# Performance work log

Hardware: AMD Instinct MI355X
Metric: run time of the kernel (lower is better)

Reference implementation:

```python
import jax, jax.numpy as jnp
import numpy as np

B = 4
G = 1024                      # GridSize
H = 1.0 / (G - 1)             # h = (right-left)/(GridSize-1), area=[[0,0],[1,1]]
GD = 0.0                      # boundary value for hard_encode padding


def _cross(a):
    # sum of 4-neighborhood: matches conv2d with kernel [[0,.5,0],[.5,0,.5],[0,.5,0]] / 0.5
    return a[..., :-2, 1:-1] + a[..., 2:, 1:-1] + a[..., 1:-1, :-2] + a[..., 1:-1, 2:]


def _inner(a):
    return a[..., 1:-1, 1:-1]


def kappa(x, mu):
    # assumed parameterization (kappa undefined in source): exp(mu * x)
    return jnp.exp(mu * x)


def setup_inputs() -> dict:
    key = jax.random.key(0)
    k1, k2, k3, k4 = jax.random.split(key, 4)
    pre = jax.random.normal(k1, (B, 1, G - 2, G - 2), jnp.float32)
    f = jax.random.normal(k2, (B, 1, G, G), jnp.float32)
    mu = jax.random.uniform(k3, (1,), jnp.float32)
    prev_pre = jax.random.normal(k4, (B, 1, G, G), jnp.float32) * 0.1
    return {"pre": pre, "f": f, "mu": mu, "prev_pre": prev_pre, "maxiter": 20}


def reference(pre, f, mu, prev_pre, maxiter):
    # w = kappa(prev_pre, mu) is iteration-invariant -> hoist out of the loop
    w = kappa(prev_pre, mu)            # [B,1,G,G]
    w_in = _inner(w)                   # [B,1,G-2,G-2]
    force = _inner(f) * (H * H)
    # k3 conv: 0.5*cross + 2*center
    y3 = 0.5 * _cross(w) + 2.0 * w_in

    def step(y, _):
        u = jnp.pad(y, ((0, 0), (0, 0), (1, 1), (1, 1)), constant_values=GD)
        y1 = 0.5 * _cross(u) * w_in    # conv(u, k1) * w_inner
        y2 = 0.5 * _cross(w * u)       # conv(w*u, k2)
        return (force + y1 + y2) / y3, None

    # original: one jac_step, then `maxiter` more -> maxiter+1 total
    y, _ = jax.lax.scan(step, pre, None, length=maxiter + 1)
    return y
```

## Files before the change

### kernel.cpp

```cpp
#include <hip/hip_runtime.h>

#define BB 4
#define GG 1024
#define NI 1022
#define SROW 1024
#define HH2 (2.0f / (1023.0f * 1023.0f))
#define OFFC 12
#define TOUTC 104
#define NTC 10

typedef float vf4 __attribute__((ext_vector_type(4)));
typedef float vf2 __attribute__((ext_vector_type(2)));

typedef __attribute__((address_space(3))) void lds_vt;
typedef const __attribute__((address_space(1))) void gm_vt;

__device__ __forceinline__ float dpp_left(float x) {
    int i = __builtin_bit_cast(int, x);
    i = __builtin_amdgcn_update_dpp(i, i, 0x138, 0xf, 0xf, false);
    return __builtin_bit_cast(float, i);
}
__device__ __forceinline__ float dpp_right(float x) {
    int i = __builtin_bit_cast(int, x);
    i = __builtin_amdgcn_update_dpp(i, i, 0x130, 0xf, 0xf, false);
    return __builtin_bit_cast(float, i);
}

#define WG_BAR() do { \
    asm volatile("s_waitcnt lgkmcnt(0)" ::: "memory"); \
    __builtin_amdgcn_s_barrier(); \
    asm volatile("" ::: "memory"); } while (0)

template<int TKP, int OFFR, int TOUTR, bool VIN4, bool VOUT4>
__global__ __launch_bounds__(512, 4)
void pinn_pipe(const float* __restrict__ ysrc,
               const float* __restrict__ fglob,
               const float* __restrict__ mu_p,
               const float* __restrict__ pp,
               float* __restrict__ yout)
{
    __shared__ __align__(16) float smem[20480];
    float* const wstg  = smem;
    float* const fstg  = smem + 8192;
    float* const ytopb = smem + 16384;
    float* const ybotb = smem + 18432;

    const int tid  = threadIdx.x;
    const int tx   = tid & 31, ty = tid >> 5;
    const int wvid = tid >> 6;
    const int ln   = tid & 63;
    const int b    = blockIdx.z;
    const int AR   = blockIdx.y * TOUTR - OFFR;
    const int R    = 4 * ty, c0 = 4 * tx;
    const float mu = mu_p[0];
    const size_t pb = (size_t)b * GG * GG;
    const int X    = AR + R;

    auto stage = [&](int A0) {
        const int scol = min(max(A0 + (ln & 31) * 4, 0), GG - 4);
        #pragma unroll
        for (int i = 0; i < 4; ++i) {
            const int j = (i * 8 + wvid) * 2 + (ln >> 5);
            const int g = min(max(AR + 1 + j, 0), GG - 1);
            const size_t go = pb + (size_t)g * GG + scol;
            __builtin_amdgcn_global_load_lds((gm_vt*)&pp[go],
                (lds_vt*)(wstg + (i * 8 + wvid) * 256), 16, 0, 0);
            __builtin_amdgcn_global_load_lds((gm_vt*)&fglob[go],
                (lds_vt*)(fstg + (i * 8 + wvid) * 256), 16, 0, 0);
        }
    };

    stage(2 * blockIdx.x * TOUTC - OFFC);

    const int tyo = ty * 128 + c0;
    const int upo = max(ty - 1, 0)  * 128 + c0;
    const int dno = min(ty + 1, 15) * 128 + c0;

    for (int tt = 0; tt < 2; ++tt) {
        const int A0 = (2 * blockIdx.x + tt) * TOUTC - OFFC;

        vf4 y0v, y1v, y2v, y3v;
        {
            const int i0 = min(max(X,     0), NI - 1);
            const int i1 = min(max(X + 1, 0), NI - 1);
            const int i2 = min(max(X + 2, 0), NI - 1);
            const int i3 = min(max(X + 3, 0), NI - 1);
            if (VIN4) {
                const int cy = min(max(A0 + c0, 0), SROW - 4);
                y0v = *(const vf4*)&ysrc[(size_t)(b * NI + i0) * SROW + cy];
                y1v = *(const vf4*)&ysrc[(size_t)(b * NI + i1) * SROW + cy];
                y2v = *(const vf4*)&ysrc[(size_t)(b * NI + i2) * SROW + cy];
                y3v = *(const vf4*)&ysrc[(size_t)(b * NI + i3) * SROW + cy];
            } else {
                const int cy  = min(max(A0 + c0, 0), NI - 2);
                const int cy2 = min(cy + 2, NI - 2);
                #define LDY(dst, ii) { \
                    const size_t base_ = (size_t)(b * NI + (ii)) * NI; \
                    const vf2 a_ = *(const vf2*)&ysrc[base_ + cy]; \
                    const vf2 b_ = *(const vf2*)&ysrc[base_ + cy2]; \
                    dst[0] = a_[0]; dst[1] = a_[1]; dst[2] = b_[0]; dst[3] = b_[1]; }
                LDY(y0v, i0) LDY(y1v, i1) LDY(y2v, i2) LDY(y3v, i3)
                #undef LDY
            }
        }

        __syncthreads();

        #pragma unroll
        for (int u = 0; u < 4; ++u) {
            vf4 w = *(const vf4*)&wstg[(R + u) * 128 + c0];
            #pragma unroll
            for (int m = 0; m < 4; ++m) w[m] = __expf(mu * w[m]);
            *(vf4*)&wstg[(R + u) * 128 + c0] = w;
        }
        __syncthreads();

        vf4 bN0,bS0,bW0,bE0,bf0, bN1,bS1,bW1,bE1,bf1,
            bN2,bS2,bW2,bE2,bf2, bN3,bS3,bW3,bE3,bf3;

        #define COEFF(kk, BN, BS, BW, BE, BF, YV) { \
            const int jN = max(R + (kk) - 1, 0); \
            const int jC = R + (kk); \
            const int jS = min(R + (kk) + 1, 63); \
            const int ce = min(c0 + 4, 124); \
            const vf4 n4 = *(const vf4*)&wstg[jN * 128 + c0]; \
            const vf2 n2 = *(const vf2*)&wstg[jN * 128 + ce]; \
            const vf4 c4 = *(const vf4*)&wstg[jC * 128 + c0]; \
            const vf2 c2 = *(const vf2*)&wstg[jC * 128 + ce]; \
            const vf4 s4 = *(const vf4*)&wstg[jS * 128 + c0]; \
            const vf2 s2 = *(const vf2*)&wstg[jS * 128 + ce]; \
            const vf4 wN = {n4[1], n4[2], n4[3], n2[0]}; \
            const vf4 wW = c4; \
            const vf4 wC = {c4[1], c4[2], c4[3], c2[0]}; \
            const vf4 wE = {c4[2], c4[3], c2[0], c2[1]}; \
            const vf4 wS = {s4[1], s4[2], s4[3], s2[0]}; \
            const vf4 aN = wC + wN, aS = wC + wS, aW = wC + wW, aE = wC + wE; \
            const vf4 den = (aN + aS) + (aW + aE); \
            const int gi = X + (kk); \
            vf4 rd; \
            _Pragma("unroll") \
            for (int m = 0; m < 4; ++m) { \
                float x = __builtin_amdgcn_rcpf(den[m]); \
                x = x * (2.0f - den[m] * x); \
                const int gj = A0 + c0 + m; \
                const bool in = (gi >= 0) && (gi < NI) && (gj >= 0) && (gj < NI); \
                rd[m] = in ? x : 0.0f; \
                YV[m] = in ? YV[m] : 0.0f; \
            } \
            BN = aN * rd; BS = aS * rd; BW = aW * rd; BE = aE * rd; \
            const vf4 f4 = *(const vf4*)&fstg[jC * 128 + c0]; \
            const float f1 = fstg[jC * 128 + min(c0 + 4, 127)]; \
            const vf4 fC = {f4[1], f4[2], f4[3], f1}; \
            BF = (fC * rd) * HH2; }

        COEFF(0, bN0,bS0,bW0,bE0,bf0, y0v)
        COEFF(1, bN1,bS1,bW1,bE1,bf1, y1v)
        COEFF(2, bN2,bS2,bW2,bE2,bf2, y2v)
        COEFF(3, bN3,bS3,bW3,bE3,bf3, y3v)
        #undef COEFF

        __syncthreads();

        if (tt == 0) stage((2 * blockIdx.x + 1) * TOUTC - OFFC);

        for (int t = 1; t <= TKP; ++t) {
            *(vf4*)&ytopb[tyo] = y0v;
            *(vf4*)&ybotb[tyo] = y3v;
            WG_BAR();
            const vf4 up = *(const vf4*)&ybotb[upo];
            const vf4 dn = *(const vf4*)&ytopb[dno];
            WG_BAR();
            const vf4 yW0 = {dpp_left(y0v[3]), y0v[0], y0v[1], y0v[2]};
            const vf4 yW1 = {dpp_left(y1v[3]), y1v[0], y1v[1], y1v[2]};
            const vf4 yW2 = {dpp_left(y2v[3]), y2v[0], y2v[1], y2v[2]};
            const vf4 yW3 = {dpp_left(y3v[3]), y3v[0], y3v[1], y3v[2]};
            const vf4 yE0 = {y0v[1], y0v[2], y0v[3], dpp_right(y0v[0])};
            const vf4 yE1 = {y1v[1], y1v[2], y1v[3], dpp_right(y1v[0])};
            const vf4 yE2 = {y2v[1], y2v[2], y2v[3], dpp_right(y2v[0])};
            const vf4 yE3 = {y3v[1], y3v[2], y3v[3], dpp_right(y3v[0])};
            vf4 n0 = bf0; n0 += bN0 * up;  n0 += bS0 * y1v; n0 += bW0 * yW0; n0 += bE0 * yE0;
            vf4 n1 = bf1; n1 += bN1 * y0v; n1 += bS1 * y2v; n1 += bW1 * yW1; n1 += bE1 * yE1;
            vf4 n2 = bf2; n2 += bN2 * y1v; n2 += bS2 * y3v; n2 += bW2 * yW2; n2 += bE2 * yE2;
            vf4 n3 = bf3; n3 += bN3 * y2v; n3 += bS3 * dn;  n3 += bW3 * yW3; n3 += bE3 * yE3;
            y0v = n0; y1v = n1; y2v = n2; y3v = n3;
        }

        if (c0 >= OFFC && c0 < OFFC + TOUTC) {
            const int gj0 = A0 + c0;
            if (VOUT4) {
                #define STORE4(kk, YV) { \
                    const int r = R + (kk); \
                    if (r >= OFFR && r < OFFR + TOUTR) { \
                        const int gi = AR + r; \
                        if (gi < NI && gj0 <= SROW - 4) \
                            *(vf4*)&yout[(size_t)(b * NI + gi) * SROW + gj0] = YV; } }
                STORE4(0, y0v) STORE4(1, y1v) STORE4(2, y2v) STORE4(3, y3v)
                #undef STORE4
            } else {
                #define STORE(kk, YV) { \
                    const int r = R + (kk); \
                    if (r >= OFFR && r < OFFR + TOUTR) { \
                        const int gi = AR + r; \
                        if (gi < NI) { \
                            const size_t rb = (size_t)(b * NI + gi) * NI; \
                            if (gj0 + 3 < NI) { \
                                vf2 pa, pv; pa[0]=YV[0]; pa[1]=YV[1]; pv[0]=YV[2]; pv[1]=YV[3]; \
                                *(vf2*)&yout[rb + gj0] = pa; *(vf2*)&yout[rb + gj0 + 2] = pv; \
                            } else { \
                                _Pragma("unroll") \
                                for (int m = 0; m < 4; ++m) \
                                    if (gj0 + m < NI) yout[rb + gj0 + m] = YV[m]; \
                            } \
                        } } }
                STORE(0, y0v) STORE(1, y1v) STORE(2, y2v) STORE(3, y3v)
                #undef STORE
            }
        }
    }
}

extern "C" void kernel_launch(void* const* d_in, const int* in_sizes, int n_in,
                              void* d_out, int out_size, void* d_ws, size_t ws_size,
                              hipStream_t stream) {
    const float* pre = (const float*)d_in[0];
    const float* f   = (const float*)d_in[1];
    const float* mu  = (const float*)d_in[2];
    const float* pp  = (const float*)d_in[3];

    float* yA = (float*)d_ws;

    const dim3 bs(512, 1, 1);
    pinn_pipe<11, 11, 42, false, true ><<<dim3(NTC/2, 25, BB), bs, 0, stream>>>(pre, f, mu, pp, yA);
    pinn_pipe<10, 10, 44, true,  false><<<dim3(NTC/2, 24, BB), bs, 0, stream>>>(yA,  f, mu, pp, (float*)d_out);
}
```

Before: 172.9 us.

## Compute exp coefficients in registers and recompute east coefficient per step

Removes the separate LDS pass that exponentiated the staged w tile and its extra barrier. Each thread now reads its own w rows, computes exp locally, and gets the neighbouring column through DPP lane shifts; the w staging is shifted by one row so the north row lines up. The east coefficient is no longer held in registers but rebuilt every iteration as mask minus the other three, which cuts four vf4 registers at the cost of extra ALU work in the hot loop. Exp is now computed redundantly for overlapping rows, and the iteration loop is reordered so fewer temporaries are live at once.

```diff
diff --git a/kernel.cpp b/kernel.cpp
--- a/kernel.cpp
+++ b/kernel.cpp
@@ -60,12 +60,14 @@
         const int scol = min(max(A0 + (ln & 31) * 4, 0), GG - 4);
         #pragma unroll
         for (int i = 0; i < 4; ++i) {
-            const int j = (i * 8 + wvid) * 2 + (ln >> 5);
-            const int g = min(max(AR + 1 + j, 0), GG - 1);
-            const size_t go = pb + (size_t)g * GG + scol;
-            __builtin_amdgcn_global_load_lds((gm_vt*)&pp[go],
+            const int j  = (i * 8 + wvid) * 2 + (ln >> 5);
+            const int gp = min(max(AR + j,     0), GG - 1);
+            const int gf = min(max(AR + 1 + j, 0), GG - 1);
+            __builtin_amdgcn_global_load_lds(
+                (gm_vt*)&pp[pb + (size_t)gp * GG + scol],
                 (lds_vt*)(wstg + (i * 8 + wvid) * 256), 16, 0, 0);
-            __builtin_amdgcn_global_load_lds((gm_vt*)&fglob[go],
+            __builtin_amdgcn_global_load_lds(
+                (gm_vt*)&fglob[pb + (size_t)gf * GG + scol],
                 (lds_vt*)(fstg + (i * 8 + wvid) * 256), 16, 0, 0);
         }
     };
@@ -76,8 +78,18 @@
     const int upo = max(ty - 1, 0)  * 128 + c0;
     const int dno = min(ty + 1, 15) * 128 + c0;
 
+    vf4 rmv;
+    #pragma unroll
+    for (int k = 0; k < 4; ++k)
+        rmv[k] = ((unsigned)(X + k) < (unsigned)NI) ? 1.0f : 0.0f;
+
     for (int tt = 0; tt < 2; ++tt) {
         const int A0 = (2 * blockIdx.x + tt) * TOUTC - OFFC;
+
+        vf4 colm;
+        #pragma unroll
+        for (int m = 0; m < 4; ++m)
+            colm[m] = ((unsigned)(A0 + c0 + m) < (unsigned)NI) ? 1.0f : 0.0f;
 
         vf4 y0v, y1v, y2v, y3v;
         {
@@ -106,57 +118,52 @@
 
         __syncthreads();
 
-        #pragma unroll
-        for (int u = 0; u < 4; ++u) {
-            vf4 w = *(const vf4*)&wstg[(R + u) * 128 + c0];
-            #pragma unroll
-            for (int m = 0; m < 4; ++m) w[m] = __expf(mu * w[m]);
-            *(vf4*)&wstg[(R + u) * 128 + c0] = w;
-        }
-        __syncthreads();
-
-        vf4 bN0,bS0,bW0,bE0,bf0, bN1,bS1,bW1,bE1,bf1,
-            bN2,bS2,bW2,bE2,bf2, bN3,bS3,bW3,bE3,bf3;
-
-        #define COEFF(kk, BN, BS, BW, BE, BF, YV) { \
-            const int jN = max(R + (kk) - 1, 0); \
-            const int jC = R + (kk); \
-            const int jS = min(R + (kk) + 1, 63); \
-            const int ce = min(c0 + 4, 124); \
-            const vf4 n4 = *(const vf4*)&wstg[jN * 128 + c0]; \
-            const vf2 n2 = *(const vf2*)&wstg[jN * 128 + ce]; \
-            const vf4 c4 = *(const vf4*)&wstg[jC * 128 + c0]; \
-            const vf2 c2 = *(const vf2*)&wstg[jC * 128 + ce]; \
-            const vf4 s4 = *(const vf4*)&wstg[jS * 128 + c0]; \
-            const vf2 s2 = *(const vf2*)&wstg[jS * 128 + ce]; \
-            const vf4 wN = {n4[1], n4[2], n4[3], n2[0]}; \
-            const vf4 wW = c4; \
-            const vf4 wC = {c4[1], c4[2], c4[3], c2[0]}; \
-            const vf4 wE = {c4[2], c4[3], c2[0], c2[1]}; \
-            const vf4 wS = {s4[1], s4[2], s4[3], s2[0]}; \
+        vf4 bN0,bS0,bW0,bf0, bN1,bS1,bW1,bf1,
+            bN2,bS2,bW2,bf2, bN3,bS3,bW3,bf3;
+
+        #define COEFF(kk, BN, BS, BW, BF, YV) { \
+            const int jN = R + (kk); \
+            const int jC = min(R + (kk) + 1, 63); \
+            const int jS = min(R + (kk) + 2, 63); \
+            vf4 wNr = *(const volatile vf4*)&wstg[jN * 128 + c0]; \
+            vf4 wCr = *(const volatile vf4*)&wstg[jC * 128 + c0]; \
+            vf4 wSr = *(const volatile vf4*)&wstg[jS * 128 + c0]; \
+            const vf4 fr = *(const volatile vf4*)&fstg[jN * 128 + c0]; \
+            _Pragma("unroll") \
+            for (int m = 0; m < 4; ++m) { \
+                wNr[m] = __expf(mu * wNr[m]); \
+                wCr[m] = __expf(mu * wCr[m]); \
+                wSr[m] = __expf(mu * wSr[m]); \
+            } \
+            const float s1N = dpp_right(wNr[0]); \
+            const float s1C = dpp_right(wCr[0]); \
+            const float s1S = dpp_right(wSr[0]); \
+            const float s2C = dpp_right(wCr[1]); \
+            const float SF  = dpp_right(fr[0]); \
+            const vf4 wN = {wNr[1], wNr[2], wNr[3], s1N}; \
+            const vf4 wW = wCr; \
+            const vf4 wC = {wCr[1], wCr[2], wCr[3], s1C}; \
+            const vf4 wE = {wCr[2], wCr[3], s1C, s2C}; \
+            const vf4 wS = {wSr[1], wSr[2], wSr[3], s1S}; \
             const vf4 aN = wC + wN, aS = wC + wS, aW = wC + wW, aE = wC + wE; \
             const vf4 den = (aN + aS) + (aW + aE); \
-            const int gi = X + (kk); \
             vf4 rd; \
             _Pragma("unroll") \
             for (int m = 0; m < 4; ++m) { \
                 float x = __builtin_amdgcn_rcpf(den[m]); \
                 x = x * (2.0f - den[m] * x); \
-                const int gj = A0 + c0 + m; \
-                const bool in = (gi >= 0) && (gi < NI) && (gj >= 0) && (gj < NI); \
+                const bool in = (rmv[(kk)] != 0.0f) && (colm[m] != 0.0f); \
                 rd[m] = in ? x : 0.0f; \
                 YV[m] = in ? YV[m] : 0.0f; \
             } \
-            BN = aN * rd; BS = aS * rd; BW = aW * rd; BE = aE * rd; \
-            const vf4 f4 = *(const vf4*)&fstg[jC * 128 + c0]; \
-            const float f1 = fstg[jC * 128 + min(c0 + 4, 127)]; \
-            const vf4 fC = {f4[1], f4[2], f4[3], f1}; \
+            BN = aN * rd; BS = aS * rd; BW = aW * rd; \
+            const vf4 fC = {fr[1], fr[2], fr[3], SF}; \
             BF = (fC * rd) * HH2; }
 
-        COEFF(0, bN0,bS0,bW0,bE0,bf0, y0v)
-        COEFF(1, bN1,bS1,bW1,bE1,bf1, y1v)
-        COEFF(2, bN2,bS2,bW2,bE2,bf2, y2v)
-        COEFF(3, bN3,bS3,bW3,bE3,bf3, y3v)
+        COEFF(0, bN0,bS0,bW0,bf0, y0v)
+        COEFF(1, bN1,bS1,bW1,bf1, y1v)
+        COEFF(2, bN2,bS2,bW2,bf2, y2v)
+        COEFF(3, bN3,bS3,bW3,bf3, y3v)
         #undef COEFF
 
         __syncthreads();
@@ -170,19 +177,26 @@
             const vf4 up = *(const vf4*)&ybotb[upo];
             const vf4 dn = *(const vf4*)&ytopb[dno];
             WG_BAR();
+
             const vf4 yW0 = {dpp_left(y0v[3]), y0v[0], y0v[1], y0v[2]};
+            const vf4 yE0 = {y0v[1], y0v[2], y0v[3], dpp_right(y0v[0])};
+            const vf4 bE0 = ((colm * rmv[0]) - bN0 - bS0) - bW0;
+            vf4 t0 = bf0; t0 += bN0 * up;  t0 += bS0 * y1v; t0 += bW0 * yW0; t0 += bE0 * yE0;
             const vf4 yW1 = {dpp_left(y1v[3]), y1v[0], y1v[1], y1v[2]};
+            const vf4 yE1 = {y1v[1], y1v[2], y1v[3], dpp_right(y1v[0])};
+            const vf4 bE1 = ((colm * rmv[1]) - bN1 - bS1) - bW1;
+            vf4 t1 = bf1; t1 += bN1 * y0v; t1 += bS1 * y2v; t1 += bW1 * yW1; t1 += bE1 * yE1;
+            y0v = t0;
             const vf4 yW2 = {dpp_left(y2v[3]), y2v[0], y2v[1], y2v[2]};
+            const vf4 yE2 = {y2v[1], y2v[2], y2v[3], dpp_right(y2v[0])};
+            const vf4 bE2 = ((colm * rmv[2]) - bN2 - bS2) - bW2;
+            vf4 t2 = bf2; t2 += bN2 * y1v; t2 += bS2 * y3v; t2 += bW2 * yW2; t2 += bE2 * yE2;
+            y1v = t1;
             const vf4 yW3 = {dpp_left(y3v[3]), y3v[0], y3v[1], y3v[2]};
-            const vf4 yE0 = {y0v[1], y0v[2], y0v[3], dpp_right(y0v[0])};
-            const vf4 yE1 = {y1v[1], y1v[2], y1v[3], dpp_right(y1v[0])};
-            const vf4 yE2 = {y2v[1], y2v[2], y2v[3], dpp_right(y2v[0])};
             const vf4 yE3 = {y3v[1], y3v[2], y3v[3], dpp_right(y3v[0])};
-            vf4 n0 = bf0; n0 += bN0 * up;  n0 += bS0 * y1v; n0 += bW0 * yW0; n0 += bE0 * yE0;
-            vf4 n1 = bf1; n1 += bN1 * y0v; n1 += bS1 * y2v; n1 += bW1 * yW1; n1 += bE1 * yE1;
-            vf4 n2 = bf2; n2 += bN2 * y1v; n2 += bS2 * y3v; n2 += bW2 * yW2; n2 += bE2 * yE2;
-            vf4 n3 = bf3; n3 += bN3 * y2v; n3 += bS3 * dn;  n3 += bW3 * yW3; n3 += bE3 * yE3;
-            y0v = n0; y1v = n1; y2v = n2; y3v = n3;
+            const vf4 bE3 = ((colm * rmv[3]) - bN3 - bS3) - bW3;
+            vf4 t3 = bf3; t3 += bN3 * y2v; t3 += bS3 * dn;  t3 += bW3 * yW3; t3 += bE3 * yE3;
+            y2v = t2; y3v = t3;
         }
 
         if (c0 >= OFFC && c0 < OFFC + TOUTC) {
```

New measurement: 199.2 us. +15.2%, slower.
